# Optimization experiments

Measured on AMD Instinct MI355X. Metric: run time of the kernel, lower is better.

## Reference

```python
import jax, jax.numpy as jnp
import numpy as np

B, T, E, H = 64, 512, 512, 512


def _gru_scan(x_tbe, h0, Wz, bz, Wr, br, Wh, bh):
    # x_tbe: [T, B, E]; h0: [B, H]
    def step(h, x_t):
        combined = jnp.concatenate([x_t, h], axis=1)          # [B, E+H]
        z = jax.nn.sigmoid(combined @ Wz.T + bz)
        r = jax.nn.sigmoid(combined @ Wr.T + br)
        combined_reset = jnp.concatenate([x_t, r * h], axis=1)
        h_t = jnp.tanh(combined_reset @ Wh.T + bh)
        h_new = (1.0 - z) * h + z * h_t
        return h_new, h_new
    h_last, outs = jax.lax.scan(step, h0, x_tbe)
    return outs, h_last  # outs: [T, B, H]


def setup_inputs() -> dict:
    key = jax.random.key(0)
    ks = jax.random.split(key, 4)
    s = 1.0 / np.sqrt(E + H)
    return {
        "x": jax.random.normal(ks[0], (B, T, E), dtype=jnp.float32),
        "hidden_state": jnp.zeros((B, H), dtype=jnp.float32),
        "Wz": jax.random.normal(ks[1], (H, E + H), dtype=jnp.float32) * s,
        "bz": jnp.zeros((H,), dtype=jnp.float32),
        "Wr": jax.random.normal(ks[2], (H, E + H), dtype=jnp.float32) * s,
        "br": jnp.zeros((H,), dtype=jnp.float32),
        "Wh": jax.random.normal(ks[3], (H, E + H), dtype=jnp.float32) * s,
        "bh": jnp.zeros((H,), dtype=jnp.float32),
    }


def reference(x, hidden_state, Wz, bz, Wr, br, Wh, bh):
    x_tbe = jnp.swapaxes(x, 0, 1)  # [T, B, E]
    out_f, _ = _gru_scan(x_tbe, hidden_state, Wz, bz, Wr, br, Wh, bh)
    # backward direction: reverse time, scan, reverse outputs
    out_b_rev, _ = _gru_scan(x_tbe[::-1], hidden_state, Wz, bz, Wr, br, Wh, bh)
    out_b = out_b_rev[::-1]
    out = jnp.swapaxes(out_f + out_b, 0, 1)  # mode='sum', [B, T, H]
    return out, hidden_state
```

## Files before the change

### kernel.cpp

```cpp
#include <hip/hip_runtime.h>
#include <stdint.h>

#define BDIM 64
#define TDIM 512
#define EDIM 512
#define HDIM 512

typedef __attribute__((ext_vector_type(8))) short bf16x8;
typedef __attribute__((ext_vector_type(4))) float f32x4;
typedef __attribute__((ext_vector_type(4))) unsigned int u32x4;
typedef __attribute__((ext_vector_type(4))) unsigned short u16x4;
typedef unsigned long long u64t;

static __device__ __forceinline__ unsigned short f2bf(float f) {
  union { float f; uint32_t u; } c; c.f = f;
  uint32_t u = c.u;
  uint32_t r = u + 0x7fffu + ((u >> 16) & 1u);
  return (unsigned short)(r >> 16);
}
static __device__ __forceinline__ float bf2f(unsigned short s) {
  union { uint32_t u; float f; } c; c.u = ((uint32_t)s) << 16;
  return c.f;
}

#define SWZ(row, byteInRow) ((((row)*1024) + (byteInRow)) ^ ((((row)&7))<<4))
#define SWZA(row, byteInRow) ((((row)*128) + (byteInRow)) ^ ((((row)&7))<<4))


__global__ void sentinel_kern(float* out, int n) {
  for (int i = blockIdx.x * blockDim.x + threadIdx.x; i < n; i += gridDim.x * blockDim.x)
    out[i] = -12345.0f;
}

__global__ void conv_w(const float* __restrict__ Wz, const float* __restrict__ Wr,
                       const float* __restrict__ Wh,
                       unsigned short* __restrict__ Wxb, unsigned short* __restrict__ Whb) {
  int idx = blockIdx.x * 256 + threadIdx.x;
  if (idx >= 3 * 512 * 1024) return;
  int g = idx >> 19;
  int rem = idx & 524287;
  int j = rem >> 10, k = rem & 1023;
  const float* W = (g == 0) ? Wz : (g == 1) ? Wr : Wh;
  unsigned short b = f2bf(W[(size_t)j * 1024 + k]);
  if (k < 512) Wxb[((size_t)g * 512 + j) * 512 + k] = b;
  else         Whb[((size_t)g * 512 + j) * 512 + (k - 512)] = b;
}

__global__ void conv_x(const float* __restrict__ x, unsigned short* __restrict__ xb, int n4) {
  for (int i = blockIdx.x * blockDim.x + threadIdx.x; i < n4; i += gridDim.x * blockDim.x) {
    f32x4 v = ((const f32x4*)x)[i];
    u16x4 o;
    o[0] = f2bf(v[0]); o[1] = f2bf(v[1]); o[2] = f2bf(v[2]); o[3] = f2bf(v[3]);
    ((u16x4*)xb)[i] = o;
  }
}

__global__ void add_out(float* __restrict__ out, const float* __restrict__ Hb, int n4) {
  for (int i = blockIdx.x * blockDim.x + threadIdx.x; i < n4; i += gridDim.x * blockDim.x) {
    f32x4 a = ((const f32x4*)out)[i];
    f32x4 b = ((const f32x4*)Hb)[i];
    ((f32x4*)out)[i] = a + b;
  }
}


__global__ __launch_bounds__(256, 2)
void gru_xproj(const unsigned short* __restrict__ xb,
               const unsigned short* __restrict__ Wxb,
               const float* __restrict__ bz, const float* __restrict__ br,
               const float* __restrict__ bh,
               unsigned short* __restrict__ Gb) {
  __shared__ __align__(16) unsigned short lA[128 * 64];
  __shared__ __align__(16) unsigned short lB[128 * 64];
  const int tid = threadIdx.x;
  const int m0 = blockIdx.x * 128;
  const int n0 = blockIdx.y * 128;
  const int w = tid >> 6, lane = tid & 63, cl = lane & 15, q = lane >> 4;
  const int wr = w >> 1, wc = w & 1;
  f32x4 acc[4][4];
#pragma unroll
  for (int i = 0; i < 4; i++)
#pragma unroll
    for (int j = 0; j < 4; j++) acc[i][j] = (f32x4){0.f, 0.f, 0.f, 0.f};

  for (int ko = 0; ko < 8; ko++) {
    int k0 = ko * 64;
#pragma unroll
    for (int cc = 0; cc < 4; cc++) {
      int qq = tid * 4 + cc;
      int row = qq >> 3, kc = qq & 7;
      u32x4 va = *(const u32x4*)(xb + ((size_t)(m0 + row) * EDIM + k0 + kc * 8));
      *(u32x4*)((char*)lA + SWZA(row, kc * 16)) = va;
      u32x4 vb = *(const u32x4*)(Wxb + ((size_t)(n0 + row) * EDIM + k0 + kc * 8));
      *(u32x4*)((char*)lB + SWZA(row, kc * 16)) = vb;
    }
    __syncthreads();
#pragma unroll
    for (int ks = 0; ks < 2; ks++) {
      bf16x8 af[4], bfv[4];
#pragma unroll
      for (int i = 0; i < 4; i++) {
        int rl = wr * 64 + i * 16 + cl;
        af[i] = *(const bf16x8*)((char*)lA + SWZA(rl, ks * 64 + q * 16));
      }
#pragma unroll
      for (int j = 0; j < 4; j++) {
        int rl = wc * 64 + j * 16 + cl;
        bfv[j] = *(const bf16x8*)((char*)lB + SWZA(rl, ks * 64 + q * 16));
      }
#pragma unroll
      for (int i = 0; i < 4; i++)
#pragma unroll
        for (int j = 0; j < 4; j++)
          acc[i][j] = __builtin_amdgcn_mfma_f32_16x16x32_bf16(af[i], bfv[j], acc[i][j], 0, 0, 0);
    }
    __syncthreads();
  }
  const int g = n0 >> 9;
  const float* bias = (g == 0) ? bz : (g == 1) ? br : bh;
#pragma unroll
  for (int i = 0; i < 4; i++) {
#pragma unroll
    for (int j = 0; j < 4; j++) {
      int n = n0 + wc * 64 + j * 16 + cl;
      float bv = bias[n & 511];
#pragma unroll
      for (int ii = 0; ii < 4; ii++) {
        int m = m0 + wr * 64 + i * 16 + q * 4 + ii;
        Gb[(size_t)m * 1536 + n] = f2bf(acc[i][j][ii] + bv);
      }
    }
  }
}


__device__ __forceinline__ void gbar(unsigned int* ctr, unsigned int& ep, int tid) {
  asm volatile("s_waitcnt vmcnt(0)" ::: "memory");
  __syncthreads();
  if (tid == 0) {
    ep++;
    unsigned int target = ep * 16u;
    __hip_atomic_fetch_add(ctr, 1u, __ATOMIC_RELAXED, __HIP_MEMORY_SCOPE_AGENT);
    while (__hip_atomic_load(ctr, __ATOMIC_RELAXED, __HIP_MEMORY_SCOPE_AGENT) < target) {}
  }
  __syncthreads();
}

__global__ __launch_bounds__(256, 1)
void gru_persist(const unsigned short* __restrict__ Gb,
                 const float* __restrict__ h0,
                 unsigned short* __restrict__ Hst,
                 unsigned short* __restrict__ RHst,
                 unsigned int*   __restrict__ ctrs,
                 float* __restrict__ outp,
                 float* __restrict__ Hb,
                 const unsigned short* __restrict__ Whb) {
  __shared__ __align__(16) unsigned short lds_w[6 * 16 * 512];
  __shared__ __align__(16) unsigned short lds_ah[16 * 512];
  __shared__ __align__(16) unsigned short lds_arh[16 * 512];
  __shared__ float lds_hprev[16 * 32];

  const int tid = threadIdx.x;
  const int bid = blockIdx.x;
  const int gid = bid & 7;
  const int cg = bid >> 3;
  const int dir = gid >> 2;
  const int bg = gid & 3;
  const int j0 = cg * 32;
  const int w = tid >> 6;
  const int lane = tid & 63;
  const int c = lane & 15;
  const int q = lane >> 4;
  unsigned int* ctr = &ctrs[gid * 32];

  for (int qk = tid; qk < 6144; qk += 256) {
    int nt = qk >> 10;
    int cin = qk & 1023;
    int col = cin & 15;
    int kc = cin >> 4;
    int g = nt >> 1, sub2 = nt & 1;
    int jglob = j0 + sub2 * 16 + col;
    u32x4 v = *(const u32x4*)(Whb + (((size_t)g * 512 + jglob) * 512 + kc * 8));
    *(u32x4*)((char*)lds_w + nt * 16384 + SWZ(col, kc * 16)) = v;
  }

#pragma unroll
  for (int ii = 0; ii < 2; ii++) {
    int idx = tid * 2 + ii;
    int row = idx >> 5, jl = idx & 31;
    int b = bg * 16 + row, j = j0 + jl;
    float v = h0[(size_t)b * HDIM + j];
    lds_hprev[row * 32 + jl] = v;
    __hip_atomic_store(&Hst[((size_t)dir * 64 + b) * 512 + j], f2bf(v),
                       __ATOMIC_RELAXED, __HIP_MEMORY_SCOPE_AGENT);
  }

  unsigned int ep = 0;
  gbar(ctr, ep, tid);

  const int sub = w & 1;
  const int jn = j0 + sub * 16 + c;
  const int gateA = (w < 2) ? 0 : 1;

  for (int s = 0; s < TDIM; s++) {
    int t = dir ? (TDIM - 1 - s) : s;

    f32x4 gA, gC;
#pragma unroll
    for (int i = 0; i < 4; i++) {
      int b = bg * 16 + q * 4 + i;
      size_t mrow = (size_t)b * TDIM + t;
      size_t giA = (mrow * 3 + gateA) * HDIM + jn;
      gA[i] = bf2f(Gb[giA]);
      if (w < 2) {
        size_t giC = (mrow * 3 + 2) * HDIM + jn;
        gC[i] = bf2f(Gb[giC]);
      }
    }

    {
      int row = tid >> 4, seg = tid & 15;
      const char* srcb = (const char*)Hst +
                         (size_t)(dir * 64 + bg * 16 + row) * 1024 + seg * 8;
      u64t v[8];
#pragma unroll
      for (int i = 0; i < 8; i++)
        v[i] = __hip_atomic_load((const u64t*)(srcb + i * 128),
                                 __ATOMIC_RELAXED, __HIP_MEMORY_SCOPE_AGENT);
      char* dst = (char*)lds_ah;
#pragma unroll
      for (int i = 0; i < 8; i++)
        *(u64t*)(dst + SWZ(row, seg * 8 + i * 128)) = v[i];
    }
    __syncthreads();

    f32x4 a0 = (f32x4){0.f,0.f,0.f,0.f}, a1 = (f32x4){0.f,0.f,0.f,0.f};
    f32x4 a2 = (f32x4){0.f,0.f,0.f,0.f}, a3 = (f32x4){0.f,0.f,0.f,0.f};
    {
      const char* wb = (const char*)lds_w + w * 16384;
      const char* ab = (const char*)lds_ah;
#pragma unroll
      for (int ks = 0; ks < 4; ks++) {
#pragma unroll
        for (int p = 0; p < 4; p++) {
          int kb = (ks * 4 + p) * 64 + q * 16;
          bf16x8 af = *(const bf16x8*)(ab + SWZ(c, kb));
          bf16x8 bfv = *(const bf16x8*)(wb + SWZ(c, kb));
          if (p == 0) a0 = __builtin_amdgcn_mfma_f32_16x16x32_bf16(af, bfv, a0, 0, 0, 0);
          else if (p == 1) a1 = __builtin_amdgcn_mfma_f32_16x16x32_bf16(af, bfv, a1, 0, 0, 0);
          else if (p == 2) a2 = __builtin_amdgcn_mfma_f32_16x16x32_bf16(af, bfv, a2, 0, 0, 0);
          else a3 = __builtin_amdgcn_mfma_f32_16x16x32_bf16(af, bfv, a3, 0, 0, 0);
        }
      }
    }
    f32x4 acc = (a0 + a1) + (a2 + a3);
    f32x4 zreg;
    if (w < 2) {
#pragma unroll
      for (int i = 0; i < 4; i++) {
        float pre = acc[i] + gA[i];
        pre = fminf(fmaxf(pre, -30.f), 30.f);
        zreg[i] = 1.f / (1.f + __expf(-pre));
      }
    } else {
      float rhv[4];
#pragma unroll
      for (int i = 0; i < 4; i++) {
        int row = q * 4 + i;
        float pre = acc[i] + gA[i];
        pre = fminf(fmaxf(pre, -30.f), 30.f);
        float sg = 1.f / (1.f + __expf(-pre));
        rhv[i] = sg * lds_hprev[row * 32 + sub * 16 + c];
      }
#pragma unroll
      for (int i = 0; i < 4; i++) {
        float oth = __shfl_xor(rhv[i], 1);
        if (!(c & 1)) {
          int b = bg * 16 + q * 4 + i;
          unsigned int pk = (unsigned int)f2bf(rhv[i]) | ((unsigned int)f2bf(oth) << 16);
          __hip_atomic_store(
              (unsigned int*)&RHst[(size_t)(dir * 64 + b) * 512 + jn],
              pk, __ATOMIC_RELAXED, __HIP_MEMORY_SCOPE_AGENT);
        }
      }
    }
    gbar(ctr, ep, tid);

    {
      int row = tid >> 4, seg = tid & 15;
      const char* srcb = (const char*)RHst +
                         (size_t)(dir * 64 + bg * 16 + row) * 1024 + seg * 8;
      u64t v[8];
#pragma unroll
      for (int i = 0; i < 8; i++)
        v[i] = __hip_atomic_load((const u64t*)(srcb + i * 128),
                                 __ATOMIC_RELAXED, __HIP_MEMORY_SCOPE_AGENT);
      char* dst = (char*)lds_arh;
#pragma unroll
      for (int i = 0; i < 8; i++)
        *(u64t*)(dst + SWZ(row, seg * 8 + i * 128)) = v[i];
    }
    __syncthreads();

    if (w < 2) {
      f32x4 b0 = (f32x4){0.f,0.f,0.f,0.f}, b1 = (f32x4){0.f,0.f,0.f,0.f};
      f32x4 b2 = (f32x4){0.f,0.f,0.f,0.f}, b3 = (f32x4){0.f,0.f,0.f,0.f};
      const char* wb = (const char*)lds_w + (4 + sub) * 16384;
      const char* ab = (const char*)lds_arh;
#pragma unroll
      for (int ks = 0; ks < 4; ks++) {
#pragma unroll
        for (int p = 0; p < 4; p++) {
          int kb = (ks * 4 + p) * 64 + q * 16;
          bf16x8 af = *(const bf16x8*)(ab + SWZ(c, kb));
          bf16x8 bfv = *(const bf16x8*)(wb + SWZ(c, kb));
          if (p == 0) b0 = __builtin_amdgcn_mfma_f32_16x16x32_bf16(af, bfv, b0, 0, 0, 0);
          else if (p == 1) b1 = __builtin_amdgcn_mfma_f32_16x16x32_bf16(af, bfv, b1, 0, 0, 0);
          else if (p == 2) b2 = __builtin_amdgcn_mfma_f32_16x16x32_bf16(af, bfv, b2, 0, 0, 0);
          else b3 = __builtin_amdgcn_mfma_f32_16x16x32_bf16(af, bfv, b3, 0, 0, 0);
        }
      }
      f32x4 acc2 = (b0 + b1) + (b2 + b3);
      float* op = dir ? Hb : outp;
      float hn[4];
#pragma unroll
      for (int i = 0; i < 4; i++) {
        int row = q * 4 + i;
        int b = bg * 16 + row;
        float pre = acc2[i] + gC[i];
        pre = fminf(fmaxf(pre, -15.f), 15.f);
        float e2 = __expf(2.f * pre);
        float th = (e2 - 1.f) / (e2 + 1.f);
        float hp = lds_hprev[row * 32 + sub * 16 + c];
        float z = zreg[i];
        hn[i] = hp + z * (th - hp);
        op[((size_t)b * TDIM + t) * HDIM + jn] = hn[i];
        lds_hprev[row * 32 + sub * 16 + c] = hn[i];
      }
#pragma unroll
      for (int i = 0; i < 4; i++) {
        float oth = __shfl_xor(hn[i], 1);
        if (!(c & 1)) {
          int b = bg * 16 + q * 4 + i;
          unsigned int pk = (unsigned int)f2bf(hn[i]) | ((unsigned int)f2bf(oth) << 16);
          __hip_atomic_store(
              (unsigned int*)&Hst[(size_t)(dir * 64 + b) * 512 + jn],
              pk, __ATOMIC_RELAXED, __HIP_MEMORY_SCOPE_AGENT);
        }
      }
    }
    gbar(ctr, ep, tid);
  }
}


extern "C" void kernel_launch(void* const* d_in, const int* in_sizes, int n_in,
                              void* d_out, int out_size, void* d_ws, size_t ws_size,
                              hipStream_t stream) {
  (void)in_sizes; (void)n_in;
  const float* x  = (const float*)d_in[0];
  const float* h0 = (const float*)d_in[1];
  const float* Wz = (const float*)d_in[2];
  const float* bz = (const float*)d_in[3];
  const float* Wr = (const float*)d_in[4];
  const float* br = (const float*)d_in[5];
  const float* Wh = (const float*)d_in[6];
  const float* bh = (const float*)d_in[7];
  float* outp = (float*)d_out;

  const size_t szG    = (size_t)32768 * 1536 * 2;
  const size_t szXb   = (size_t)BDIM * TDIM * EDIM * 2;
  const size_t szW    = (size_t)3 * 512 * 512 * 2;
  const size_t szHb   = (size_t)BDIM * TDIM * HDIM * 4;
  const size_t szHst  = (size_t)2 * 64 * 512 * 2;
  const size_t szFl   = 4096;
  const size_t fixed  = szXb + 2 * szW + szHb + 2 * szHst + szFl + 16384;

  if (ws_size < fixed + szG) {
    sentinel_kern<<<256, 256, 0, stream>>>(outp, out_size);
    return;
  }

  size_t off = 0;
  char* base = (char*)d_ws;
  auto alloc = [&](size_t sz) { char* p = base + off; off = (off + sz + 255) & ~(size_t)255; return p; };
  unsigned short* Gb   = (unsigned short*)alloc(szG);
  unsigned short* xb   = (unsigned short*)alloc(szXb);
  unsigned short* Wxb  = (unsigned short*)alloc(szW);
  unsigned short* Whb  = (unsigned short*)alloc(szW);
  float*          Hbuf = (float*)alloc(szHb);
  unsigned short* Hst  = (unsigned short*)alloc(szHst);
  unsigned short* RHst = (unsigned short*)alloc(szHst);
  unsigned int*   ctrs = (unsigned int*)alloc(szFl);

  hipMemsetAsync(ctrs, 0, szFl, stream);
  conv_w<<<(3 * 512 * 1024 + 255) / 256, 256, 0, stream>>>(Wz, Wr, Wh, Wxb, Whb);
  conv_x<<<2048, 256, 0, stream>>>(x, xb, (BDIM * TDIM * EDIM) / 4);
  gru_xproj<<<dim3(256, 12), 256, 0, stream>>>(xb, Wxb, bz, br, bh, Gb);
  gru_persist<<<128, 256, 0, stream>>>(Gb, h0, Hst, RHst, ctrs, outp, Hbuf, Whb);
  add_out<<<2048, 256, 0, stream>>>(outp, Hbuf, (BDIM * TDIM * HDIM) / 4);
  hipMemcpyAsync(outp + (size_t)BDIM * TDIM * HDIM, h0,
                 (size_t)BDIM * HDIM * sizeof(float), hipMemcpyDeviceToDevice, stream);
}
```

Baseline: 2.946 ms.

## Process both GRU directions per block with interleaved split-phase barriers

Each persistent block now handles both forward and backward directions for its batch group and column slice, halving the grid. Global barriers are split into separate arrive and wait on per-direction, per-phase counters, so one direction's barrier latency can be hidden behind the other direction's compute. This doubles per-block work per step and uses more counters, trading parallelism for latency hiding.

```diff
diff --git a/kernel.cpp b/kernel.cpp
--- a/kernel.cpp
+++ b/kernel.cpp
@@ -134,18 +134,6 @@
 }
 
 
-__device__ __forceinline__ void gbar(unsigned int* ctr, unsigned int& ep, int tid) {
-  asm volatile("s_waitcnt vmcnt(0)" ::: "memory");
-  __syncthreads();
-  if (tid == 0) {
-    ep++;
-    unsigned int target = ep * 16u;
-    __hip_atomic_fetch_add(ctr, 1u, __ATOMIC_RELAXED, __HIP_MEMORY_SCOPE_AGENT);
-    while (__hip_atomic_load(ctr, __ATOMIC_RELAXED, __HIP_MEMORY_SCOPE_AGENT) < target) {}
-  }
-  __syncthreads();
-}
-
 __global__ __launch_bounds__(256, 1)
 void gru_persist(const unsigned short* __restrict__ Gb,
                  const float* __restrict__ h0,
@@ -156,22 +144,24 @@
                  float* __restrict__ Hb,
                  const unsigned short* __restrict__ Whb) {
   __shared__ __align__(16) unsigned short lds_w[6 * 16 * 512];
-  __shared__ __align__(16) unsigned short lds_ah[16 * 512];
-  __shared__ __align__(16) unsigned short lds_arh[16 * 512];
-  __shared__ float lds_hprev[16 * 32];
+  __shared__ __align__(16) unsigned short lds_st[2][16 * 512];
+  __shared__ float lds_hp[2][16 * 32];
 
   const int tid = threadIdx.x;
   const int bid = blockIdx.x;
-  const int gid = bid & 7;
-  const int cg = bid >> 3;
-  const int dir = gid >> 2;
-  const int bg = gid & 3;
+  const int bg = bid & 3;
+  const int cg = bid >> 2;
   const int j0 = cg * 32;
   const int w = tid >> 6;
   const int lane = tid & 63;
   const int c = lane & 15;
   const int q = lane >> 4;
-  unsigned int* ctr = &ctrs[gid * 32];
+  const int sub = w & 1;
+  const int jn = j0 + sub * 16 + c;
+  const int gateA = (w < 2) ? 0 : 1;
+
+  unsigned int* ctr_rh[2] = { &ctrs[(0 * 4 + bg) * 32], &ctrs[(4 + bg) * 32] };
+  unsigned int* ctr_h[2]  = { &ctrs[(8 + 0 * 4 + bg) * 32], &ctrs[(8 + 4 + bg) * 32] };
 
   for (int qk = tid; qk < 6144; qk += 256) {
     int nt = qk >> 10;
@@ -185,82 +175,75 @@
   }
 
 #pragma unroll
-  for (int ii = 0; ii < 2; ii++) {
-    int idx = tid * 2 + ii;
-    int row = idx >> 5, jl = idx & 31;
-    int b = bg * 16 + row, j = j0 + jl;
-    float v = h0[(size_t)b * HDIM + j];
-    lds_hprev[row * 32 + jl] = v;
-    __hip_atomic_store(&Hst[((size_t)dir * 64 + b) * 512 + j], f2bf(v),
-                       __ATOMIC_RELAXED, __HIP_MEMORY_SCOPE_AGENT);
-  }
-
-  unsigned int ep = 0;
-  gbar(ctr, ep, tid);
-
-  const int sub = w & 1;
-  const int jn = j0 + sub * 16 + c;
-  const int gateA = (w < 2) ? 0 : 1;
-
-  for (int s = 0; s < TDIM; s++) {
-    int t = dir ? (TDIM - 1 - s) : s;
-
-    f32x4 gA, gC;
-#pragma unroll
-    for (int i = 0; i < 4; i++) {
-      int b = bg * 16 + q * 4 + i;
-      size_t mrow = (size_t)b * TDIM + t;
-      size_t giA = (mrow * 3 + gateA) * HDIM + jn;
-      gA[i] = bf2f(Gb[giA]);
-      if (w < 2) {
-        size_t giC = (mrow * 3 + 2) * HDIM + jn;
-        gC[i] = bf2f(Gb[giC]);
-      }
-    }
-
-    {
-      int row = tid >> 4, seg = tid & 15;
-      const char* srcb = (const char*)Hst +
-                         (size_t)(dir * 64 + bg * 16 + row) * 1024 + seg * 8;
-      u64t v[8];
-#pragma unroll
-      for (int i = 0; i < 8; i++)
-        v[i] = __hip_atomic_load((const u64t*)(srcb + i * 128),
-                                 __ATOMIC_RELAXED, __HIP_MEMORY_SCOPE_AGENT);
-      char* dst = (char*)lds_ah;
-#pragma unroll
-      for (int i = 0; i < 8; i++)
-        *(u64t*)(dst + SWZ(row, seg * 8 + i * 128)) = v[i];
-    }
-    __syncthreads();
-
+  for (int d = 0; d < 2; d++) {
+#pragma unroll
+    for (int ii = 0; ii < 2; ii++) {
+      int idx = tid * 2 + ii;
+      int row = idx >> 5, jl = idx & 31;
+      int b = bg * 16 + row, j = j0 + jl;
+      float v = h0[(size_t)b * HDIM + j];
+      lds_hp[d][row * 32 + jl] = v;
+      __hip_atomic_store(&Hst[((size_t)d * 64 + b) * 512 + j], f2bf(v),
+                         __ATOMIC_RELAXED, __HIP_MEMORY_SCOPE_AGENT);
+    }
+  }
+  asm volatile("s_waitcnt vmcnt(0)" ::: "memory");
+  __syncthreads();
+  if (tid == 0) {
+    __hip_atomic_fetch_add(ctr_h[0], 1u, __ATOMIC_RELAXED, __HIP_MEMORY_SCOPE_AGENT);
+    __hip_atomic_fetch_add(ctr_h[1], 1u, __ATOMIC_RELAXED, __HIP_MEMORY_SCOPE_AGENT);
+  }
+
+  auto garrive = [&](unsigned int* ctr) {
+    asm volatile("s_waitcnt vmcnt(0)" ::: "memory");
+    __syncthreads();
+    if (tid == 0)
+      __hip_atomic_fetch_add(ctr, 1u, __ATOMIC_RELAXED, __HIP_MEMORY_SCOPE_AGENT);
+  };
+  auto gwait = [&](unsigned int* ctr, unsigned tgt) {
+    if (tid == 0)
+      while (__hip_atomic_load(ctr, __ATOMIC_RELAXED, __HIP_MEMORY_SCOPE_AGENT) < tgt) {}
+    __syncthreads();
+  };
+  auto stage = [&](const unsigned short* srcArr, int d, unsigned short* dstLds) {
+    int row = tid >> 4, seg = tid & 15;
+    const char* srcb = (const char*)srcArr + (size_t)(d * 64 + bg * 16 + row) * 1024 + seg * 8;
+    u64t v[8];
+#pragma unroll
+    for (int i = 0; i < 8; i++)
+      v[i] = __hip_atomic_load((const u64t*)(srcb + i * 128),
+                               __ATOMIC_RELAXED, __HIP_MEMORY_SCOPE_AGENT);
+    char* dst = (char*)dstLds;
+#pragma unroll
+    for (int i = 0; i < 8; i++)
+      *(u64t*)(dst + SWZ(row, seg * 8 + i * 128)) = v[i];
+  };
+  auto mfma16 = [&](const char* ab, const char* wb) -> f32x4 {
     f32x4 a0 = (f32x4){0.f,0.f,0.f,0.f}, a1 = (f32x4){0.f,0.f,0.f,0.f};
     f32x4 a2 = (f32x4){0.f,0.f,0.f,0.f}, a3 = (f32x4){0.f,0.f,0.f,0.f};
-    {
-      const char* wb = (const char*)lds_w + w * 16384;
-      const char* ab = (const char*)lds_ah;
-#pragma unroll
-      for (int ks = 0; ks < 4; ks++) {
-#pragma unroll
-        for (int p = 0; p < 4; p++) {
-          int kb = (ks * 4 + p) * 64 + q * 16;
-          bf16x8 af = *(const bf16x8*)(ab + SWZ(c, kb));
-          bf16x8 bfv = *(const bf16x8*)(wb + SWZ(c, kb));
-          if (p == 0) a0 = __builtin_amdgcn_mfma_f32_16x16x32_bf16(af, bfv, a0, 0, 0, 0);
-          else if (p == 1) a1 = __builtin_amdgcn_mfma_f32_16x16x32_bf16(af, bfv, a1, 0, 0, 0);
-          else if (p == 2) a2 = __builtin_amdgcn_mfma_f32_16x16x32_bf16(af, bfv, a2, 0, 0, 0);
-          else a3 = __builtin_amdgcn_mfma_f32_16x16x32_bf16(af, bfv, a3, 0, 0, 0);
-        }
-      }
-    }
-    f32x4 acc = (a0 + a1) + (a2 + a3);
-    f32x4 zreg;
+#pragma unroll
+    for (int ks = 0; ks < 4; ks++) {
+#pragma unroll
+      for (int p = 0; p < 4; p++) {
+        int kb = (ks * 4 + p) * 64 + q * 16;
+        bf16x8 af = *(const bf16x8*)(ab + SWZ(c, kb));
+        bf16x8 bfv = *(const bf16x8*)(wb + SWZ(c, kb));
+        if (p == 0) a0 = __builtin_amdgcn_mfma_f32_16x16x32_bf16(af, bfv, a0, 0, 0, 0);
+        else if (p == 1) a1 = __builtin_amdgcn_mfma_f32_16x16x32_bf16(af, bfv, a1, 0, 0, 0);
+        else if (p == 2) a2 = __builtin_amdgcn_mfma_f32_16x16x32_bf16(af, bfv, a2, 0, 0, 0);
+        else a3 = __builtin_amdgcn_mfma_f32_16x16x32_bf16(af, bfv, a3, 0, 0, 0);
+      }
+    }
+    return (a0 + a1) + (a2 + a3);
+  };
+  auto P1 = [&](int d, const char* ab, const f32x4& gA, f32x4& zreg_s) {
+    f32x4 acc = mfma16(ab, (const char*)lds_w + w * 16384);
     if (w < 2) {
 #pragma unroll
       for (int i = 0; i < 4; i++) {
         float pre = acc[i] + gA[i];
         pre = fminf(fmaxf(pre, -30.f), 30.f);
-        zreg[i] = 1.f / (1.f + __expf(-pre));
+        zreg_s[i] = 1.f / (1.f + __expf(-pre));
       }
     } else {
       float rhv[4];
@@ -270,7 +253,7 @@
         float pre = acc[i] + gA[i];
         pre = fminf(fmaxf(pre, -30.f), 30.f);
         float sg = 1.f / (1.f + __expf(-pre));
-        rhv[i] = sg * lds_hprev[row * 32 + sub * 16 + c];
+        rhv[i] = sg * lds_hp[d][row * 32 + sub * 16 + c];
       }
 #pragma unroll
       for (int i = 0; i < 4; i++) {
@@ -279,49 +262,16 @@
           int b = bg * 16 + q * 4 + i;
           unsigned int pk = (unsigned int)f2bf(rhv[i]) | ((unsigned int)f2bf(oth) << 16);
           __hip_atomic_store(
-              (unsigned int*)&RHst[(size_t)(dir * 64 + b) * 512 + jn],
+              (unsigned int*)&RHst[(size_t)(d * 64 + b) * 512 + jn],
               pk, __ATOMIC_RELAXED, __HIP_MEMORY_SCOPE_AGENT);
         }
       }
     }
-    gbar(ctr, ep, tid);
-
-    {
-      int row = tid >> 4, seg = tid & 15;
-      const char* srcb = (const char*)RHst +
-                         (size_t)(dir * 64 + bg * 16 + row) * 1024 + seg * 8;
-      u64t v[8];
-#pragma unroll
-      for (int i = 0; i < 8; i++)
-        v[i] = __hip_atomic_load((const u64t*)(srcb + i * 128),
-                                 __ATOMIC_RELAXED, __HIP_MEMORY_SCOPE_AGENT);
-      char* dst = (char*)lds_arh;
-#pragma unroll
-      for (int i = 0; i < 8; i++)
-        *(u64t*)(dst + SWZ(row, seg * 8 + i * 128)) = v[i];
-    }
-    __syncthreads();
-
+  };
+  auto P2 = [&](int d, const char* ab, const f32x4& gC, const f32x4& zreg_s,
+                float* op, int t) {
     if (w < 2) {
-      f32x4 b0 = (f32x4){0.f,0.f,0.f,0.f}, b1 = (f32x4){0.f,0.f,0.f,0.f};
-      f32x4 b2 = (f32x4){0.f,0.f,0.f,0.f}, b3 = (f32x4){0.f,0.f,0.f,0.f};
-      const char* wb = (const char*)lds_w + (4 + sub) * 16384;
-      const char* ab = (const char*)lds_arh;
-#pragma unroll
-      for (int ks = 0; ks < 4; ks++) {
-#pragma unroll
-        for (int p = 0; p < 4; p++) {
-          int kb = (ks * 4 + p) * 64 + q * 16;
-          bf16x8 af = *(const bf16x8*)(ab + SWZ(c, kb));
-          bf16x8 bfv = *(const bf16x8*)(wb + SWZ(c, kb));
-          if (p == 0) b0 = __builtin_amdgcn_mfma_f32_16x16x32_bf16(af, bfv, b0, 0, 0, 0);
-          else if (p == 1) b1 = __builtin_amdgcn_mfma_f32_16x16x32_bf16(af, bfv, b1, 0, 0, 0);
-          else if (p == 2) b2 = __builtin_amdgcn_mfma_f32_16x16x32_bf16(af, bfv, b2, 0, 0, 0);
-          else b3 = __builtin_amdgcn_mfma_f32_16x16x32_bf16(af, bfv, b3, 0, 0, 0);
-        }
-      }
-      f32x4 acc2 = (b0 + b1) + (b2 + b3);
-      float* op = dir ? Hb : outp;
+      f32x4 acc2 = mfma16(ab, (const char*)lds_w + (4 + sub) * 16384);
       float hn[4];
 #pragma unroll
       for (int i = 0; i < 4; i++) {
@@ -331,11 +281,11 @@
         pre = fminf(fmaxf(pre, -15.f), 15.f);
         float e2 = __expf(2.f * pre);
         float th = (e2 - 1.f) / (e2 + 1.f);
-        float hp = lds_hprev[row * 32 + sub * 16 + c];
-        float z = zreg[i];
+        float hp = lds_hp[d][row * 32 + sub * 16 + c];
+        float z = zreg_s[i];
         hn[i] = hp + z * (th - hp);
         op[((size_t)b * TDIM + t) * HDIM + jn] = hn[i];
-        lds_hprev[row * 32 + sub * 16 + c] = hn[i];
+        lds_hp[d][row * 32 + sub * 16 + c] = hn[i];
       }
 #pragma unroll
       for (int i = 0; i < 4; i++) {
@@ -344,12 +294,57 @@
           int b = bg * 16 + q * 4 + i;
           unsigned int pk = (unsigned int)f2bf(hn[i]) | ((unsigned int)f2bf(oth) << 16);
           __hip_atomic_store(
-              (unsigned int*)&Hst[(size_t)(dir * 64 + b) * 512 + jn],
+              (unsigned int*)&Hst[(size_t)(d * 64 + b) * 512 + jn],
               pk, __ATOMIC_RELAXED, __HIP_MEMORY_SCOPE_AGENT);
         }
       }
     }
-    gbar(ctr, ep, tid);
+  };
+
+  f32x4 zreg_f, zreg_b;
+
+  for (int s = 0; s < TDIM; s++) {
+    const int t_f = s;
+    const int t_b = TDIM - 1 - s;
+    const unsigned tgt = 16u * (unsigned)(s + 1);
+
+    f32x4 gA_f, gC_f, gA_b, gC_b;
+#pragma unroll
+    for (int i = 0; i < 4; i++) {
+      int b = bg * 16 + q * 4 + i;
+      size_t mf = ((size_t)b * TDIM + t_f) * 3;
+      size_t mb = ((size_t)b * TDIM + t_b) * 3;
+      gA_f[i] = bf2f(Gb[(mf + gateA) * HDIM + jn]);
+      gA_b[i] = bf2f(Gb[(mb + gateA) * HDIM + jn]);
+      if (w < 2) {
+        gC_f[i] = bf2f(Gb[(mf + 2) * HDIM + jn]);
+        gC_b[i] = bf2f(Gb[(mb + 2) * HDIM + jn]);
+      }
+    }
+
+    gwait(ctr_h[0], tgt);
+    stage(Hst, 0, lds_st[0]);
+    __syncthreads();
+    P1(0, (const char*)lds_st[0], gA_f, zreg_f);
+    garrive(ctr_rh[0]);
+
+    gwait(ctr_h[1], tgt);
+    stage(Hst, 1, lds_st[1]);
+    __syncthreads();
+    P1(1, (const char*)lds_st[1], gA_b, zreg_b);
+    garrive(ctr_rh[1]);
+
+    gwait(ctr_rh[0], tgt);
+    stage(RHst, 0, lds_st[0]);
+    __syncthreads();
+    P2(0, (const char*)lds_st[0], gC_f, zreg_f, outp, t_f);
+    garrive(ctr_h[0]);
+
+    gwait(ctr_rh[1], tgt);
+    stage(RHst, 1, lds_st[1]);
+    __syncthreads();
+    P2(1, (const char*)lds_st[1], gC_b, zreg_b, Hb, t_b);
+    garrive(ctr_h[1]);
   }
 }
 
@@ -397,7 +392,7 @@
   conv_w<<<(3 * 512 * 1024 + 255) / 256, 256, 0, stream>>>(Wz, Wr, Wh, Wxb, Whb);
   conv_x<<<2048, 256, 0, stream>>>(x, xb, (BDIM * TDIM * EDIM) / 4);
   gru_xproj<<<dim3(256, 12), 256, 0, stream>>>(xb, Wxb, bz, br, bh, Gb);
-  gru_persist<<<128, 256, 0, stream>>>(Gb, h0, Hst, RHst, ctrs, outp, Hbuf, Whb);
+  gru_persist<<<64, 256, 0, stream>>>(Gb, h0, Hst, RHst, ctrs, outp, Hbuf, Whb);
   add_out<<<2048, 256, 0, stream>>>(outp, Hbuf, (BDIM * TDIM * HDIM) / 4);
   hipMemcpyAsync(outp + (size_t)BDIM * TDIM * HDIM, h0,
                  (size_t)BDIM * HDIM * sizeof(float), hipMemcpyDeviceToDevice, stream);
```

New measurement: 4.809 ms. +63.2%, slower.

## Replace atomic-counter grid barrier with per-block flag lines and split arrive/wait

Applied to the files above, without the earlier changes.

Replaces the shared atomic-add counter barrier with one flag line per block. Each block stores its step number after publishing its data, and one wavefront polls all 16 peer flags in parallel with s_sleep backoff. The barrier is split into arrive and wait, so the bf16 gate loads are issued before waiting on h. The fp32 output store is moved after the arrive so it no longer sits on the critical path. This is meant to cut atomic contention and serialized barrier latency in the 512-step recurrence, but it relies on relaxed-ordering flag semantics being correct.

```diff
diff --git a/kernel.cpp b/kernel.cpp
--- a/kernel.cpp
+++ b/kernel.cpp
@@ -134,24 +134,12 @@
 }
 
 
-__device__ __forceinline__ void gbar(unsigned int* ctr, unsigned int& ep, int tid) {
-  asm volatile("s_waitcnt vmcnt(0)" ::: "memory");
-  __syncthreads();
-  if (tid == 0) {
-    ep++;
-    unsigned int target = ep * 16u;
-    __hip_atomic_fetch_add(ctr, 1u, __ATOMIC_RELAXED, __HIP_MEMORY_SCOPE_AGENT);
-    while (__hip_atomic_load(ctr, __ATOMIC_RELAXED, __HIP_MEMORY_SCOPE_AGENT) < target) {}
-  }
-  __syncthreads();
-}
-
 __global__ __launch_bounds__(256, 1)
 void gru_persist(const unsigned short* __restrict__ Gb,
                  const float* __restrict__ h0,
                  unsigned short* __restrict__ Hst,
                  unsigned short* __restrict__ RHst,
-                 unsigned int*   __restrict__ ctrs,
+                 unsigned int*   __restrict__ flags,
                  float* __restrict__ outp,
                  float* __restrict__ Hb,
                  const unsigned short* __restrict__ Whb) {
@@ -171,7 +159,11 @@
   const int lane = tid & 63;
   const int c = lane & 15;
   const int q = lane >> 4;
-  unsigned int* ctr = &ctrs[gid * 32];
+
+  unsigned int* fh_base  = flags + gid * 16 * 32;
+  unsigned int* frh_base = flags + (128 + gid * 16) * 32;
+  unsigned int* fh_own   = fh_base + cg * 32;
+  unsigned int* frh_own  = frh_base + cg * 32;
 
   for (int qk = tid; qk < 6144; qk += 256) {
     int nt = qk >> 10;
@@ -194,9 +186,30 @@
     __hip_atomic_store(&Hst[((size_t)dir * 64 + b) * 512 + j], f2bf(v),
                        __ATOMIC_RELAXED, __HIP_MEMORY_SCOPE_AGENT);
   }
-
-  unsigned int ep = 0;
-  gbar(ctr, ep, tid);
+  asm volatile("s_waitcnt vmcnt(0)" ::: "memory");
+  __syncthreads();
+  if (tid == 0)
+    __hip_atomic_store(fh_own, 1u, __ATOMIC_RELAXED, __HIP_MEMORY_SCOPE_AGENT);
+
+  auto arrive = [&](unsigned int* ownLine, unsigned val) {
+    asm volatile("s_waitcnt vmcnt(0)" ::: "memory");
+    __syncthreads();
+    if (tid == 0)
+      __hip_atomic_store(ownLine, val, __ATOMIC_RELAXED, __HIP_MEMORY_SCOPE_AGENT);
+  };
+  auto wait16 = [&](unsigned int* baseLines, unsigned tgt) {
+    if (w == 0) {
+      while (true) {
+        unsigned fv = tgt;
+        if (lane < 16)
+          fv = __hip_atomic_load(baseLines + lane * 32,
+                                 __ATOMIC_RELAXED, __HIP_MEMORY_SCOPE_AGENT);
+        if (__all(fv >= tgt)) break;
+        __builtin_amdgcn_s_sleep(1);
+      }
+    }
+    __syncthreads();
+  };
 
   const int sub = w & 1;
   const int jn = j0 + sub * 16 + c;
@@ -204,6 +217,7 @@
 
   for (int s = 0; s < TDIM; s++) {
     int t = dir ? (TDIM - 1 - s) : s;
+    const unsigned tgt = (unsigned)(s + 1);
 
     f32x4 gA, gC;
 #pragma unroll
@@ -217,6 +231,8 @@
         gC[i] = bf2f(Gb[giC]);
       }
     }
+
+    wait16(fh_base, tgt);
 
     {
       int row = tid >> 4, seg = tid & 15;
@@ -284,7 +300,9 @@
         }
       }
     }
-    gbar(ctr, ep, tid);
+    arrive(frh_own, tgt);
+
+    wait16(frh_base, tgt);
 
     {
       int row = tid >> 4, seg = tid & 15;
@@ -302,6 +320,7 @@
     }
     __syncthreads();
 
+    float hn[4];
     if (w < 2) {
       f32x4 b0 = (f32x4){0.f,0.f,0.f,0.f}, b1 = (f32x4){0.f,0.f,0.f,0.f};
       f32x4 b2 = (f32x4){0.f,0.f,0.f,0.f}, b3 = (f32x4){0.f,0.f,0.f,0.f};
@@ -321,12 +340,9 @@
         }
       }
       f32x4 acc2 = (b0 + b1) + (b2 + b3);
-      float* op = dir ? Hb : outp;
-      float hn[4];
 #pragma unroll
       for (int i = 0; i < 4; i++) {
         int row = q * 4 + i;
-        int b = bg * 16 + row;
         float pre = acc2[i] + gC[i];
         pre = fminf(fmaxf(pre, -15.f), 15.f);
         float e2 = __expf(2.f * pre);
@@ -334,7 +350,6 @@
         float hp = lds_hprev[row * 32 + sub * 16 + c];
         float z = zreg[i];
         hn[i] = hp + z * (th - hp);
-        op[((size_t)b * TDIM + t) * HDIM + jn] = hn[i];
         lds_hprev[row * 32 + sub * 16 + c] = hn[i];
       }
 #pragma unroll
@@ -349,7 +364,16 @@
         }
       }
     }
-    gbar(ctr, ep, tid);
+    arrive(fh_own, tgt + 1);
+
+    if (w < 2) {
+      float* op = dir ? Hb : outp;
+#pragma unroll
+      for (int i = 0; i < 4; i++) {
+        int b = bg * 16 + q * 4 + i;
+        op[((size_t)b * TDIM + t) * HDIM + jn] = hn[i];
+      }
+    }
   }
 }
 
@@ -373,7 +397,7 @@
   const size_t szW    = (size_t)3 * 512 * 512 * 2;
   const size_t szHb   = (size_t)BDIM * TDIM * HDIM * 4;
   const size_t szHst  = (size_t)2 * 64 * 512 * 2;
-  const size_t szFl   = 4096;
+  const size_t szFl   = 32768;
   const size_t fixed  = szXb + 2 * szW + szHb + 2 * szHst + szFl + 16384;
 
   if (ws_size < fixed + szG) {
@@ -391,13 +415,13 @@
   float*          Hbuf = (float*)alloc(szHb);
   unsigned short* Hst  = (unsigned short*)alloc(szHst);
   unsigned short* RHst = (unsigned short*)alloc(szHst);
-  unsigned int*   ctrs = (unsigned int*)alloc(szFl);
-
-  hipMemsetAsync(ctrs, 0, szFl, stream);
+  unsigned int*   flags= (unsigned int*)alloc(szFl);
+
+  hipMemsetAsync(flags, 0, szFl, stream);
   conv_w<<<(3 * 512 * 1024 + 255) / 256, 256, 0, stream>>>(Wz, Wr, Wh, Wxb, Whb);
   conv_x<<<2048, 256, 0, stream>>>(x, xb, (BDIM * TDIM * EDIM) / 4);
   gru_xproj<<<dim3(256, 12), 256, 0, stream>>>(xb, Wxb, bz, br, bh, Gb);
-  gru_persist<<<128, 256, 0, stream>>>(Gb, h0, Hst, RHst, ctrs, outp, Hbuf, Whb);
+  gru_persist<<<128, 256, 0, stream>>>(Gb, h0, Hst, RHst, flags, outp, Hbuf, Whb);
   add_out<<<2048, 256, 0, stream>>>(outp, Hbuf, (BDIM * TDIM * HDIM) / 4);
   hipMemcpyAsync(outp + (size_t)BDIM * TDIM * HDIM, h0,
                  (size_t)BDIM * HDIM * sizeof(float), hipMemcpyDeviceToDevice, stream);
```

Measured after the change: 2.874 ms. -2.5%, faster.

## Replace counter barriers with epoch-tagged data flags polled per stage

Applied to the files above, without the earlier changes.

Removes the global atomic-counter barrier between recurrence stages. Each 32-bit bf16 pair is now stored with a 32-bit step tag in a 64-bit atomic word, and consumers poll until every tag matches the expected step. Buffers are double-buffered by parity so producers can run ahead one stage. The output store is moved after the state publication. This cuts the barrier round trip and the single-thread spin, at the cost of doubled communication bytes and all threads polling with sleeps.

```diff
diff --git a/kernel.cpp b/kernel.cpp
--- a/kernel.cpp
+++ b/kernel.cpp
@@ -134,24 +134,11 @@
 }
 
 
-__device__ __forceinline__ void gbar(unsigned int* ctr, unsigned int& ep, int tid) {
-  asm volatile("s_waitcnt vmcnt(0)" ::: "memory");
-  __syncthreads();
-  if (tid == 0) {
-    ep++;
-    unsigned int target = ep * 16u;
-    __hip_atomic_fetch_add(ctr, 1u, __ATOMIC_RELAXED, __HIP_MEMORY_SCOPE_AGENT);
-    while (__hip_atomic_load(ctr, __ATOMIC_RELAXED, __HIP_MEMORY_SCOPE_AGENT) < target) {}
-  }
-  __syncthreads();
-}
-
 __global__ __launch_bounds__(256, 1)
 void gru_persist(const unsigned short* __restrict__ Gb,
                  const float* __restrict__ h0,
-                 unsigned short* __restrict__ Hst,
-                 unsigned short* __restrict__ RHst,
-                 unsigned int*   __restrict__ ctrs,
+                 char* __restrict__ Hs2,
+                 char* __restrict__ RHs2,
                  float* __restrict__ outp,
                  float* __restrict__ Hb,
                  const unsigned short* __restrict__ Whb) {
@@ -171,7 +158,10 @@
   const int lane = tid & 63;
   const int c = lane & 15;
   const int q = lane >> 4;
-  unsigned int* ctr = &ctrs[gid * 32];
+
+  auto lineoff = [&](int par, int row, int cgi) -> size_t {
+    return ((((size_t)par * 2 + dir) * 4 + bg) * 16 + row) * 16 * 128 + (size_t)cgi * 128;
+  };
 
   for (int qk = tid; qk < 6144; qk += 256) {
     int nt = qk >> 10;
@@ -184,26 +174,51 @@
     *(u32x4*)((char*)lds_w + nt * 16384 + SWZ(col, kc * 16)) = v;
   }
 
-#pragma unroll
-  for (int ii = 0; ii < 2; ii++) {
-    int idx = tid * 2 + ii;
-    int row = idx >> 5, jl = idx & 31;
-    int b = bg * 16 + row, j = j0 + jl;
-    float v = h0[(size_t)b * HDIM + j];
-    lds_hprev[row * 32 + jl] = v;
-    __hip_atomic_store(&Hst[((size_t)dir * 64 + b) * 512 + j], f2bf(v),
-                       __ATOMIC_RELAXED, __HIP_MEMORY_SCOPE_AGENT);
-  }
-
-  unsigned int ep = 0;
-  gbar(ctr, ep, tid);
+  {
+    int row = tid >> 4, jl2 = (tid & 15) * 2;
+    int b = bg * 16 + row;
+    float v0 = h0[(size_t)b * HDIM + j0 + jl2];
+    float v1 = h0[(size_t)b * HDIM + j0 + jl2 + 1];
+    lds_hprev[row * 32 + jl2] = v0;
+    lds_hprev[row * 32 + jl2 + 1] = v1;
+    unsigned int pk = (unsigned int)f2bf(v0) | ((unsigned int)f2bf(v1) << 16);
+    u64t unit = ((u64t)1u << 32) | (u64t)pk;
+    __hip_atomic_store((u64t*)(Hs2 + lineoff(0, row, cg) + (size_t)(tid & 15) * 8),
+                       unit, __ATOMIC_RELAXED, __HIP_MEMORY_SCOPE_AGENT);
+  }
+  __syncthreads();
+
+  auto pollstage = [&](const char* slab, int par, unsigned expect,
+                       unsigned short* dstLds) {
+    int row = tid >> 4, seg = tid & 15;
+    const char* lb = slab + lineoff(par, row, seg);
+    u64t v[16];
+    while (true) {
+      bool ok = true;
+#pragma unroll
+      for (int k = 0; k < 16; k++) {
+        v[k] = __hip_atomic_load((const u64t*)(lb + k * 8),
+                                 __ATOMIC_RELAXED, __HIP_MEMORY_SCOPE_AGENT);
+        ok &= ((unsigned)(v[k] >> 32) == expect);
+      }
+      if (__syncthreads_and((int)ok)) break;
+      __builtin_amdgcn_s_sleep(1);
+    }
+    char* dst = (char*)dstLds;
+#pragma unroll
+    for (int k = 0; k < 8; k++) {
+      u64t dd = (u64t)(unsigned)v[2 * k] | ((u64t)(unsigned)v[2 * k + 1] << 32);
+      *(u64t*)(dst + SWZ(row, seg * 64 + k * 8)) = dd;
+    }
+    __syncthreads();
+  };
 
   const int sub = w & 1;
   const int jn = j0 + sub * 16 + c;
   const int gateA = (w < 2) ? 0 : 1;
 
-  for (int s = 0; s < TDIM; s++) {
-    int t = dir ? (TDIM - 1 - s) : s;
+  for (int s = 1; s <= TDIM; s++) {
+    int t = dir ? (TDIM - s) : (s - 1);
 
     f32x4 gA, gC;
 #pragma unroll
@@ -218,21 +233,7 @@
       }
     }
 
-    {
-      int row = tid >> 4, seg = tid & 15;
-      const char* srcb = (const char*)Hst +
-                         (size_t)(dir * 64 + bg * 16 + row) * 1024 + seg * 8;
-      u64t v[8];
-#pragma unroll
-      for (int i = 0; i < 8; i++)
-        v[i] = __hip_atomic_load((const u64t*)(srcb + i * 128),
-                                 __ATOMIC_RELAXED, __HIP_MEMORY_SCOPE_AGENT);
-      char* dst = (char*)lds_ah;
-#pragma unroll
-      for (int i = 0; i < 8; i++)
-        *(u64t*)(dst + SWZ(row, seg * 8 + i * 128)) = v[i];
-    }
-    __syncthreads();
+    pollstage(Hs2, (s - 1) & 1, (unsigned)s, lds_ah);
 
     f32x4 a0 = (f32x4){0.f,0.f,0.f,0.f}, a1 = (f32x4){0.f,0.f,0.f,0.f};
     f32x4 a2 = (f32x4){0.f,0.f,0.f,0.f}, a3 = (f32x4){0.f,0.f,0.f,0.f};
@@ -276,32 +277,19 @@
       for (int i = 0; i < 4; i++) {
         float oth = __shfl_xor(rhv[i], 1);
         if (!(c & 1)) {
-          int b = bg * 16 + q * 4 + i;
+          int row = q * 4 + i;
           unsigned int pk = (unsigned int)f2bf(rhv[i]) | ((unsigned int)f2bf(oth) << 16);
+          u64t unit = ((u64t)(unsigned)s << 32) | (u64t)pk;
           __hip_atomic_store(
-              (unsigned int*)&RHst[(size_t)(dir * 64 + b) * 512 + jn],
-              pk, __ATOMIC_RELAXED, __HIP_MEMORY_SCOPE_AGENT);
+              (u64t*)(RHs2 + lineoff(s & 1, row, cg) + (size_t)(sub * 8 + (c >> 1)) * 8),
+              unit, __ATOMIC_RELAXED, __HIP_MEMORY_SCOPE_AGENT);
         }
       }
     }
-    gbar(ctr, ep, tid);
-
-    {
-      int row = tid >> 4, seg = tid & 15;
-      const char* srcb = (const char*)RHst +
-                         (size_t)(dir * 64 + bg * 16 + row) * 1024 + seg * 8;
-      u64t v[8];
-#pragma unroll
-      for (int i = 0; i < 8; i++)
-        v[i] = __hip_atomic_load((const u64t*)(srcb + i * 128),
-                                 __ATOMIC_RELAXED, __HIP_MEMORY_SCOPE_AGENT);
-      char* dst = (char*)lds_arh;
-#pragma unroll
-      for (int i = 0; i < 8; i++)
-        *(u64t*)(dst + SWZ(row, seg * 8 + i * 128)) = v[i];
-    }
-    __syncthreads();
-
+
+    pollstage(RHs2, s & 1, (unsigned)s, lds_arh);
+
+    float hn[4];
     if (w < 2) {
       f32x4 b0 = (f32x4){0.f,0.f,0.f,0.f}, b1 = (f32x4){0.f,0.f,0.f,0.f};
       f32x4 b2 = (f32x4){0.f,0.f,0.f,0.f}, b3 = (f32x4){0.f,0.f,0.f,0.f};
@@ -321,12 +309,9 @@
         }
       }
       f32x4 acc2 = (b0 + b1) + (b2 + b3);
-      float* op = dir ? Hb : outp;
-      float hn[4];
 #pragma unroll
       for (int i = 0; i < 4; i++) {
         int row = q * 4 + i;
-        int b = bg * 16 + row;
         float pre = acc2[i] + gC[i];
         pre = fminf(fmaxf(pre, -15.f), 15.f);
         float e2 = __expf(2.f * pre);
@@ -334,22 +319,27 @@
         float hp = lds_hprev[row * 32 + sub * 16 + c];
         float z = zreg[i];
         hn[i] = hp + z * (th - hp);
-        op[((size_t)b * TDIM + t) * HDIM + jn] = hn[i];
         lds_hprev[row * 32 + sub * 16 + c] = hn[i];
       }
 #pragma unroll
       for (int i = 0; i < 4; i++) {
         float oth = __shfl_xor(hn[i], 1);
         if (!(c & 1)) {
-          int b = bg * 16 + q * 4 + i;
+          int row = q * 4 + i;
           unsigned int pk = (unsigned int)f2bf(hn[i]) | ((unsigned int)f2bf(oth) << 16);
+          u64t unit = ((u64t)(unsigned)(s + 1) << 32) | (u64t)pk;
           __hip_atomic_store(
-              (unsigned int*)&Hst[(size_t)(dir * 64 + b) * 512 + jn],
-              pk, __ATOMIC_RELAXED, __HIP_MEMORY_SCOPE_AGENT);
+              (u64t*)(Hs2 + lineoff(s & 1, row, cg) + (size_t)(sub * 8 + (c >> 1)) * 8),
+              unit, __ATOMIC_RELAXED, __HIP_MEMORY_SCOPE_AGENT);
         }
       }
-    }
-    gbar(ctr, ep, tid);
+      float* op = dir ? Hb : outp;
+#pragma unroll
+      for (int i = 0; i < 4; i++) {
+        int b = bg * 16 + q * 4 + i;
+        op[((size_t)b * TDIM + t) * HDIM + jn] = hn[i];
+      }
+    }
   }
 }
 
@@ -372,9 +362,8 @@
   const size_t szXb   = (size_t)BDIM * TDIM * EDIM * 2;
   const size_t szW    = (size_t)3 * 512 * 512 * 2;
   const size_t szHb   = (size_t)BDIM * TDIM * HDIM * 4;
-  const size_t szHst  = (size_t)2 * 64 * 512 * 2;
-  const size_t szFl   = 4096;
-  const size_t fixed  = szXb + 2 * szW + szHb + 2 * szHst + szFl + 16384;
+  const size_t szSlab = (size_t)2 * 2 * 4 * 16 * 16 * 128;
+  const size_t fixed  = szXb + 2 * szW + szHb + 2 * szSlab + 16384;
 
   if (ws_size < fixed + szG) {
     sentinel_kern<<<256, 256, 0, stream>>>(outp, out_size);
@@ -389,15 +378,15 @@
   unsigned short* Wxb  = (unsigned short*)alloc(szW);
   unsigned short* Whb  = (unsigned short*)alloc(szW);
   float*          Hbuf = (float*)alloc(szHb);
-  unsigned short* Hst  = (unsigned short*)alloc(szHst);
-  unsigned short* RHst = (unsigned short*)alloc(szHst);
-  unsigned int*   ctrs = (unsigned int*)alloc(szFl);
-
-  hipMemsetAsync(ctrs, 0, szFl, stream);
+  char*           Hs2  = (char*)alloc(szSlab);
+  char*           RHs2 = (char*)alloc(szSlab);
+
+  hipMemsetAsync(Hs2, 0, szSlab, stream);
+  hipMemsetAsync(RHs2, 0, szSlab, stream);
   conv_w<<<(3 * 512 * 1024 + 255) / 256, 256, 0, stream>>>(Wz, Wr, Wh, Wxb, Whb);
   conv_x<<<2048, 256, 0, stream>>>(x, xb, (BDIM * TDIM * EDIM) / 4);
   gru_xproj<<<dim3(256, 12), 256, 0, stream>>>(xb, Wxb, bz, br, bh, Gb);
-  gru_persist<<<128, 256, 0, stream>>>(Gb, h0, Hst, RHst, ctrs, outp, Hbuf, Whb);
+  gru_persist<<<128, 256, 0, stream>>>(Gb, h0, Hs2, RHs2, outp, Hbuf, Whb);
   add_out<<<2048, 256, 0, stream>>>(outp, Hbuf, (BDIM * TDIM * HDIM) / 4);
   hipMemcpyAsync(outp + (size_t)BDIM * TDIM * HDIM, h0,
                  (size_t)BDIM * HDIM * sizeof(float), hipMemcpyDeviceToDevice, stream);
```

Result: slower. 10.29 ms (+249.3%).
